# Optimization experiments

Hardware: AMD Instinct MI355X
Metric: run time of the kernel (lower is better)

The kernel has to match this reference:

```python
import jax, jax.numpy as jnp
import numpy as np

MAX_SIGMA = 10.0
TRUNCATE = 4.0
R = int(TRUNCATE * MAX_SIGMA + 0.5)  # 40, static max radius (scipy: int(truncate*sigma+0.5))
L = 2 * R + 1                         # 81


def _make_kernels(sigmas):
    # sigmas: [B] -> kernels [B, L], exactly matching scipy._gaussian_kernel1d
    pos = jnp.arange(-R, R + 1, dtype=sigmas.dtype)          # [L]
    r = jnp.floor(TRUNCATE * sigmas + 0.5)                   # per-sample radius
    w = jnp.exp(-0.5 * (pos[None, :] ** 2) / (sigmas[:, None] ** 2))
    w = w * (jnp.abs(pos)[None, :] <= r[:, None])            # scipy truncation
    return w / jnp.sum(w, axis=-1, keepdims=True)


def _reflect_index(n):
    # symmetric ('reflect' in scipy) boundary indices for pad width R, valid even if R > n
    i = jnp.arange(-R, n + R)
    j = jnp.mod(i, 2 * n)
    return jnp.where(j < n, j, 2 * n - 1 - j)


def _conv_last(x, k):
    # correlate along last axis with reflect boundary; x [..., n], k [L]
    n = x.shape[-1]
    xp = x[..., _reflect_index(n)]                            # [..., n+2R]
    flat = xp.reshape(-1, 1, n + 2 * R)
    out = jax.lax.conv_general_dilated(flat, k[None, None, :],
                                       window_strides=(1,), padding='VALID')
    return out.reshape(x.shape)


def _blur_one(xi, k):
    # xi: [C, H, W]; scipy gaussian_filter with scalar sigma blurs every axis
    for ax in range(xi.ndim):
        xi = jnp.moveaxis(_conv_last(jnp.moveaxis(xi, ax, -1), k), -1, ax)
    return xi


def setup_inputs() -> dict:
    key = jax.random.key(0)
    k1, _ = jax.random.split(key)
    B, C, H, W = 64, 3, 512, 512
    x = jax.random.uniform(k1, (B, C, H, W), dtype=jnp.float32)
    blur_sigmas = jnp.asarray(np.geomspace(0.5, MAX_SIGMA, 10), dtype=jnp.float32)
    fwd_steps = jax.random.randint(jax.random.fold_in(key, 1), (B,), 0, 10, dtype=jnp.int32)
    return {"x": x, "blur_sigmas": blur_sigmas, "fwd_steps": fwd_steps}


def reference(x, blur_sigmas, fwd_steps):
    sigmas = blur_sigmas[fwd_steps]          # [B]
    kernels = _make_kernels(sigmas)          # [B, L]
    return jax.vmap(_blur_one)(x, kernels)   # [B, C, H, W]
```

## Files before the change

kernel.cpp:

```cpp
#include <hip/hip_runtime.h>
#include <hip/hip_bf16.h>

#define RMAX 40
#define LK   81
#define HH   512
#define WW   512
#define CC   3
#define BB   64
#define ROWS 2

typedef unsigned short u16;
typedef __attribute__((ext_vector_type(8))) short short8;
typedef __attribute__((ext_vector_type(4))) float f32x4;

__device__ __forceinline__ u16 f2bf(float f) {
    unsigned u = __float_as_uint(f);
    u += 0x7FFFu + ((u >> 16) & 1u);
    return (u16)(u >> 16);
}
__device__ __forceinline__ float bf2f(u16 s) {
    return __uint_as_float(((unsigned)s) << 16);
}

__global__ __launch_bounds__(256) void prep_kernel(
    const float* __restrict__ sigmas10,
    const int*   __restrict__ steps,
    int*   __restrict__ rbuf,
    float* __restrict__ mbuf,
    float* __restrict__ wbuf,
    u16*   __restrict__ atab)
{
    const int b   = blockIdx.x;
    const int tid = threadIdx.x;
    const float sigma = sigmas10[steps[b]];
    int r = (int)floorf(4.0f * sigma + 0.5f);
    if (r > RMAX) r = RMAX;
    const float s2 = sigma * sigma;

    float sum = 0.0f;
    for (int p = -r; p <= r; ++p)
        sum += expf(-0.5f * (float)(p * p) / s2);
    const float inv = 1.0f / sum;

    if (tid < 128) {
        int p = tid - 56;
        float v = 0.0f;
        if (p >= -r && p <= r)
            v = expf(-0.5f * (float)(p * p) / s2) * inv;
        wbuf[b * 128 + tid] = v;
    }

    if (tid == 0) {
        rbuf[b] = r;
        float Mm[9];
        for (int i = 0; i < 9; ++i) Mm[i] = 0.0f;
        for (int p = -r; p <= r; ++p) {
            float wv = expf(-0.5f * (float)(p * p) / s2) * inv;
            for (int c = 0; c < CC; ++c) {
                int i = c + p;
                int j = ((i % 6) + 6) % 6;
                int cc = (j < 3) ? j : 5 - j;
                Mm[c * 3 + cc] += wv;
            }
        }
        for (int c = 0; c < 3; ++c)
            for (int cc = 0; cc < 3; ++cc)
                mbuf[b * 12 + c * 4 + cc] = Mm[c * 3 + cc];
    }

    u16* ab = atab + (size_t)b * 8192;
    int e = tid * 32;
    for (int ee = 0; ee < 32; ++ee, ++e) {
        int j    = e & 7;
        int lane = (e >> 3) & 63;
        int s    = e >> 9;
        int ch   = s >> 2;
        int half = (s >> 1) & 1;
        int prec = s & 1;
        int m = 32 * ch + ((lane >> 4) << 3) + j - (lane & 15) - 16 * half;
        float wfull = 0.0f;
        if (m >= 0 && m <= 2 * r) {
            int p = m - r;
            wfull = expf(-0.5f * (float)(p * p) / s2) * inv;
        }
        u16 hi = f2bf(wfull);
        u16 val = hi;
        if (prec) val = f2bf(wfull - bf2f(hi));
        ab[e] = val;
    }
}

__global__ __launch_bounds__(256) void passB_kernel(
    const float* __restrict__ x,
    const float* __restrict__ wbuf,
    const float* __restrict__ mbuf,
    const int*   __restrict__ rbuf,
    u16* __restrict__ out1)
{
    __shared__ __align__(16) float mixed[CC * ROWS][WW + 2 * RMAX];

    const int b   = blockIdx.y;
    const int h0  = blockIdx.x * ROWS;
    const int tid = threadIdx.x;
    const int r   = __builtin_amdgcn_readfirstlane(rbuf[b]);

    const float M00 = mbuf[b * 12 + 0], M01 = mbuf[b * 12 + 1], M02 = mbuf[b * 12 + 2];
    const float M10 = mbuf[b * 12 + 4], M11 = mbuf[b * 12 + 5], M12 = mbuf[b * 12 + 6];
    const float M20 = mbuf[b * 12 + 8], M21 = mbuf[b * 12 + 9], M22 = mbuf[b * 12 + 10];

    const float* xb = x + (size_t)b * CC * HH * WW + (size_t)h0 * WW;

    for (int idx = tid; idx < WW + 2 * RMAX; idx += 256) {
        int i  = idx - RMAX;
        int jm = i & (2 * WW - 1);
        int src = (jm < WW) ? jm : (2 * WW - 1 - jm);
        float a0 = __builtin_nontemporal_load(xb + src);
        float a1 = __builtin_nontemporal_load(xb + HH * WW + src);
        float a2 = __builtin_nontemporal_load(xb + 2 * HH * WW + src);
        float b0 = __builtin_nontemporal_load(xb + WW + src);
        float b1 = __builtin_nontemporal_load(xb + HH * WW + WW + src);
        float b2 = __builtin_nontemporal_load(xb + 2 * HH * WW + WW + src);
        mixed[0][idx] = M00 * a0 + M01 * a1 + M02 * a2;
        mixed[1][idx] = M00 * b0 + M01 * b1 + M02 * b2;
        mixed[2][idx] = M10 * a0 + M11 * a1 + M12 * a2;
        mixed[3][idx] = M10 * b0 + M11 * b1 + M12 * b2;
        mixed[4][idx] = M20 * a0 + M21 * a1 + M22 * a2;
        mixed[5][idx] = M20 * b0 + M21 * b1 + M22 * b2;
    }
    __syncthreads();

    const int t0    = (RMAX - r) & ~3;
    const int n4    = ((r + RMAX + 3 - t0) >> 2) + 1;
    const int kbase = (16 + t0) >> 2;
    const float4* K4 = (const float4*)(wbuf + b * 128);

#pragma unroll
    for (int k = 0; k < 3; ++k) {
        const int task = tid + 256 * k;
        const int g    = task & 127;
        const int rc   = task >> 7;
        const int w0   = g << 2;

        const int dbase = (w0 + t0) >> 2;
        const float4* D4 = (const float4*)(&mixed[rc][0]);

        float4 Wlo = K4[kbase - 1];
        float acc0 = 0.f, acc1 = 0.f, acc2 = 0.f, acc3 = 0.f;

        for (int s = 0; s < n4; ++s) {
            float4 Whi = K4[kbase + s];
            float4 D   = D4[dbase + s];
            acc0 += Whi.x * D.x; acc1 += Wlo.w * D.x; acc2 += Wlo.z * D.x; acc3 += Wlo.y * D.x;
            acc0 += Whi.y * D.y; acc1 += Whi.x * D.y; acc2 += Wlo.w * D.y; acc3 += Wlo.z * D.y;
            acc0 += Whi.z * D.z; acc1 += Whi.y * D.z; acc2 += Whi.x * D.z; acc3 += Wlo.w * D.z;
            acc0 += Whi.w * D.w; acc1 += Whi.z * D.w; acc2 += Whi.y * D.w; acc3 += Whi.x * D.w;
            Wlo = Whi;
        }

        ushort4 o;
        o.x = f2bf(acc0); o.y = f2bf(acc1); o.z = f2bf(acc2); o.w = f2bf(acc3);
        const int c = rc >> 1, row = rc & 1;
        u16* dst = out1 + ((size_t)b * CC + c) * HH * WW
                 + (size_t)(h0 + row) * WW + w0;
        *(ushort4*)dst = o;
    }
}

__device__ __forceinline__ int refl512(int i) {
    int jm = i & (2 * HH - 1);
    return (jm < HH) ? jm : (2 * HH - 1 - jm);
}

__global__ __launch_bounds__(256) void passC_kernel(
    const u16* __restrict__ in1,
    const u16* __restrict__ atab,
    const int* __restrict__ rbuf,
    float* __restrict__ out)
{
    const int tid  = threadIdx.x;
    const int lane = tid & 63;
    const int bc   = blockIdx.z;
    const int b    = bc / 3;
    const int r    = __builtin_amdgcn_readfirstlane(rbuf[b]);
    const int h0   = blockIdx.y * 32;
    const int w    = blockIdx.x * 64 + (tid >> 6) * 16 + (lane & 15);
    const int nch  = (2 * r + 63) >> 5;
    const int rowbase = h0 - r + ((lane >> 4) << 3);

    const u16* src = in1 + (size_t)bc * HH * WW + w;
    const short8* at = (const short8*)(atab + (size_t)b * 8192);

    f32x4 acc0 = {0.f, 0.f, 0.f, 0.f};
    f32x4 acc1 = {0.f, 0.f, 0.f, 0.f};

    for (int ch = 0; ch < nch; ++ch) {
        short8 bv;
#pragma unroll
        for (int j = 0; j < 8; ++j) {
            int row = refl512(rowbase + 32 * ch + j);
            bv[j] = (short)src[(size_t)row * WW];
        }
        short8 ah0 = at[(ch * 4 + 0) * 64 + lane];
        short8 al0 = at[(ch * 4 + 1) * 64 + lane];
        short8 ah1 = at[(ch * 4 + 2) * 64 + lane];
        short8 al1 = at[(ch * 4 + 3) * 64 + lane];

        acc0 = __builtin_amdgcn_mfma_f32_16x16x32_bf16(ah0, bv, acc0, 0, 0, 0);
        acc0 = __builtin_amdgcn_mfma_f32_16x16x32_bf16(al0, bv, acc0, 0, 0, 0);
        acc1 = __builtin_amdgcn_mfma_f32_16x16x32_bf16(ah1, bv, acc1, 0, 0, 0);
        acc1 = __builtin_amdgcn_mfma_f32_16x16x32_bf16(al1, bv, acc1, 0, 0, 0);
    }

    const int orow = h0 + ((lane >> 4) << 2);
    float* dst = out + (size_t)bc * HH * WW + (size_t)orow * WW + w;
#pragma unroll
    for (int q = 0; q < 4; ++q) {
        __builtin_nontemporal_store(acc0[q], dst + (size_t)q * WW);
        __builtin_nontemporal_store(acc1[q], dst + (size_t)(q + 16) * WW);
    }
}

extern "C" void kernel_launch(void* const* d_in, const int* in_sizes, int n_in,
                              void* d_out, int out_size, void* d_ws, size_t ws_size,
                              hipStream_t stream)
{
    const float* x      = (const float*)d_in[0];
    const float* sigmas = (const float*)d_in[1];
    const int*   steps  = (const int*)d_in[2];
    float*       out    = (float*)d_out;

    int*   rbuf  = (int*)d_ws;
    float* mbuf  = (float*)((char*)d_ws + 256);
    float* wbuf  = (float*)((char*)d_ws + 4096);
    u16*   atab  = (u16*)((char*)d_ws + 65536);
    u16*   inter = (u16*)((char*)d_ws + 65536 + (1 << 20));

    prep_kernel<<<64, 256, 0, stream>>>(sigmas, steps, rbuf, mbuf, wbuf, atab);

    dim3 gB(HH / ROWS, BB);
    passB_kernel<<<gB, 256, 0, stream>>>(x, wbuf, mbuf, rbuf, inter);

    dim3 gC(WW / 64, HH / 32, BB * CC);
    passC_kernel<<<gC, 256, 0, stream>>>(inter, atab, rbuf, out);
}
```

Before: 409.8 us.

## Use MFMA for horizontal pass and write transposed fp16 intermediate

Pass B's scalar FMA convolution along W becomes MFMA f16 matrix multiplies over an fp16 LDS tile of 16 rows, with XOR swizzling to avoid bank conflicts. It writes the intermediate transposed (W-major), so pass C can load 8 contiguous H samples with a single vector load instead of 8 strided gathers. The weight tables move from bf16 hi/lo split to f16 hi/lo, with the window start aligned to 8 via an offset. The risks are fp16 range and precision on the intermediate, and scattered 2-byte transposed stores in pass B.

```diff
diff --git a/kernel.cpp b/kernel.cpp
--- a/kernel.cpp
+++ b/kernel.cpp
@@ -2,32 +2,25 @@
 #include <hip/hip_bf16.h>
 
 #define RMAX 40
-#define LK   81
 #define HH   512
 #define WW   512
 #define CC   3
 #define BB   64
-#define ROWS 2
+#define HT   16
+#define LROW 640
 
 typedef unsigned short u16;
+typedef _Float16 half8 __attribute__((ext_vector_type(8)));
 typedef __attribute__((ext_vector_type(8))) short short8;
 typedef __attribute__((ext_vector_type(4))) float f32x4;
 
-__device__ __forceinline__ u16 f2bf(float f) {
-    unsigned u = __float_as_uint(f);
-    u += 0x7FFFu + ((u >> 16) & 1u);
-    return (u16)(u >> 16);
-}
-__device__ __forceinline__ float bf2f(u16 s) {
-    return __uint_as_float(((unsigned)s) << 16);
-}
+__device__ __forceinline__ u16 h2u(_Float16 h) { return __builtin_bit_cast(u16, h); }
 
 __global__ __launch_bounds__(256) void prep_kernel(
     const float* __restrict__ sigmas10,
     const int*   __restrict__ steps,
     int*   __restrict__ rbuf,
     float* __restrict__ mbuf,
-    float* __restrict__ wbuf,
     u16*   __restrict__ atab)
 {
     const int b   = blockIdx.x;
@@ -41,14 +34,6 @@
     for (int p = -r; p <= r; ++p)
         sum += expf(-0.5f * (float)(p * p) / s2);
     const float inv = 1.0f / sum;
-
-    if (tid < 128) {
-        int p = tid - 56;
-        float v = 0.0f;
-        if (p >= -r && p <= r)
-            v = expf(-0.5f * (float)(p * p) / s2) * inv;
-        wbuf[b * 128 + tid] = v;
-    }
 
     if (tid == 0) {
         rbuf[b] = r;
@@ -68,6 +53,7 @@
                 mbuf[b * 12 + c * 4 + cc] = Mm[c * 3 + cc];
     }
 
+    const int dlt = (-r) & 7;
     u16* ab = atab + (size_t)b * 8192;
     int e = tid * 32;
     for (int ee = 0; ee < 32; ++ee, ++e) {
@@ -77,30 +63,29 @@
         int ch   = s >> 2;
         int half = (s >> 1) & 1;
         int prec = s & 1;
-        int m = 32 * ch + ((lane >> 4) << 3) + j - (lane & 15) - 16 * half;
+        int m = 32 * ch + ((lane >> 4) << 3) + j - (lane & 15) - 16 * half - dlt;
         float wfull = 0.0f;
         if (m >= 0 && m <= 2 * r) {
             int p = m - r;
             wfull = expf(-0.5f * (float)(p * p) / s2) * inv;
         }
-        u16 hi = f2bf(wfull);
-        u16 val = hi;
-        if (prec) val = f2bf(wfull - bf2f(hi));
-        ab[e] = val;
-    }
-}
-
-__global__ __launch_bounds__(256) void passB_kernel(
+        _Float16 hi = (_Float16)wfull;
+        _Float16 val = prec ? (_Float16)(wfull - (float)hi) : hi;
+        ab[e] = h2u(val);
+    }
+}
+
+__global__ __launch_bounds__(512) void passB_kernel(
     const float* __restrict__ x,
-    const float* __restrict__ wbuf,
+    const u16*   __restrict__ atab,
     const float* __restrict__ mbuf,
     const int*   __restrict__ rbuf,
-    u16* __restrict__ out1)
-{
-    __shared__ __align__(16) float mixed[CC * ROWS][WW + 2 * RMAX];
+    u16* __restrict__ interT)
+{
+    __shared__ __align__(16) u16 mixs[CC][HT][LROW];
 
     const int b   = blockIdx.y;
-    const int h0  = blockIdx.x * ROWS;
+    const int h0  = blockIdx.x * HT;
     const int tid = threadIdx.x;
     const int r   = __builtin_amdgcn_readfirstlane(rbuf[b]);
 
@@ -110,59 +95,58 @@
 
     const float* xb = x + (size_t)b * CC * HH * WW + (size_t)h0 * WW;
 
-    for (int idx = tid; idx < WW + 2 * RMAX; idx += 256) {
-        int i  = idx - RMAX;
-        int jm = i & (2 * WW - 1);
+    for (int idx = tid; idx < HT * LROW; idx += 512) {
+        int h  = idx / LROW;
+        int wi = idx - h * LROW;
+        int lw = wi - RMAX;
+        int jm = lw & (2 * WW - 1);
         int src = (jm < WW) ? jm : (2 * WW - 1 - jm);
-        float a0 = __builtin_nontemporal_load(xb + src);
-        float a1 = __builtin_nontemporal_load(xb + HH * WW + src);
-        float a2 = __builtin_nontemporal_load(xb + 2 * HH * WW + src);
-        float b0 = __builtin_nontemporal_load(xb + WW + src);
-        float b1 = __builtin_nontemporal_load(xb + HH * WW + WW + src);
-        float b2 = __builtin_nontemporal_load(xb + 2 * HH * WW + WW + src);
-        mixed[0][idx] = M00 * a0 + M01 * a1 + M02 * a2;
-        mixed[1][idx] = M00 * b0 + M01 * b1 + M02 * b2;
-        mixed[2][idx] = M10 * a0 + M11 * a1 + M12 * a2;
-        mixed[3][idx] = M10 * b0 + M11 * b1 + M12 * b2;
-        mixed[4][idx] = M20 * a0 + M21 * a1 + M22 * a2;
-        mixed[5][idx] = M20 * b0 + M21 * b1 + M22 * b2;
+        const float* px = xb + (size_t)h * WW + src;
+        float a0 = __builtin_nontemporal_load(px);
+        float a1 = __builtin_nontemporal_load(px + HH * WW);
+        float a2 = __builtin_nontemporal_load(px + 2 * HH * WW);
+        int sw = wi ^ ((h & 7) << 3);
+        mixs[0][h][sw] = h2u((_Float16)(M00 * a0 + M01 * a1 + M02 * a2));
+        mixs[1][h][sw] = h2u((_Float16)(M10 * a0 + M11 * a1 + M12 * a2));
+        mixs[2][h][sw] = h2u((_Float16)(M20 * a0 + M21 * a1 + M22 * a2));
     }
     __syncthreads();
 
-    const int t0    = (RMAX - r) & ~3;
-    const int n4    = ((r + RMAX + 3 - t0) >> 2) + 1;
-    const int kbase = (16 + t0) >> 2;
-    const float4* K4 = (const float4*)(wbuf + b * 128);
-
+    const int dlt  = (-r) & 7;
+    const int nch  = (2 * r + dlt + 63) >> 5;
+    const int lane = tid & 63;
+    const int wv   = tid >> 6;
+    const int col  = lane & 15;
+    const int g    = lane >> 4;
+    const half8* at = (const half8*)(atab + (size_t)b * 8192);
+
+    for (int task = wv; task < 48; task += 8) {
+        const int c  = task >> 4;
+        const int w0 = (task & 15) << 5;
+        const int s0w = (w0 + RMAX - r) & ~7;
+        const u16* lrow = &mixs[c][col][0];
+
+        f32x4 acc0 = {0.f, 0.f, 0.f, 0.f};
+        f32x4 acc1 = {0.f, 0.f, 0.f, 0.f};
+        for (int ch = 0; ch < nch; ++ch) {
+            int wi = (s0w + 32 * ch + 8 * g) ^ ((col & 7) << 3);
+            half8 bv  = *(const half8*)(lrow + wi);
+            half8 ah0 = at[(ch * 4 + 0) * 64 + lane];
+            half8 al0 = at[(ch * 4 + 1) * 64 + lane];
+            half8 ah1 = at[(ch * 4 + 2) * 64 + lane];
+            half8 al1 = at[(ch * 4 + 3) * 64 + lane];
+            acc0 = __builtin_amdgcn_mfma_f32_16x16x32_f16(ah0, bv, acc0, 0, 0, 0);
+            acc0 = __builtin_amdgcn_mfma_f32_16x16x32_f16(al0, bv, acc0, 0, 0, 0);
+            acc1 = __builtin_amdgcn_mfma_f32_16x16x32_f16(ah1, bv, acc1, 0, 0, 0);
+            acc1 = __builtin_amdgcn_mfma_f32_16x16x32_f16(al1, bv, acc1, 0, 0, 0);
+        }
+        u16* orow = interT + (((size_t)b * CC + c) * WW + (w0 + 4 * g)) * HH
+                  + h0 + col;
 #pragma unroll
-    for (int k = 0; k < 3; ++k) {
-        const int task = tid + 256 * k;
-        const int g    = task & 127;
-        const int rc   = task >> 7;
-        const int w0   = g << 2;
-
-        const int dbase = (w0 + t0) >> 2;
-        const float4* D4 = (const float4*)(&mixed[rc][0]);
-
-        float4 Wlo = K4[kbase - 1];
-        float acc0 = 0.f, acc1 = 0.f, acc2 = 0.f, acc3 = 0.f;
-
-        for (int s = 0; s < n4; ++s) {
-            float4 Whi = K4[kbase + s];
-            float4 D   = D4[dbase + s];
-            acc0 += Whi.x * D.x; acc1 += Wlo.w * D.x; acc2 += Wlo.z * D.x; acc3 += Wlo.y * D.x;
-            acc0 += Whi.y * D.y; acc1 += Whi.x * D.y; acc2 += Wlo.w * D.y; acc3 += Wlo.z * D.y;
-            acc0 += Whi.z * D.z; acc1 += Whi.y * D.z; acc2 += Whi.x * D.z; acc3 += Wlo.w * D.z;
-            acc0 += Whi.w * D.w; acc1 += Whi.z * D.w; acc2 += Whi.y * D.w; acc3 += Whi.x * D.w;
-            Wlo = Whi;
-        }
-
-        ushort4 o;
-        o.x = f2bf(acc0); o.y = f2bf(acc1); o.z = f2bf(acc2); o.w = f2bf(acc3);
-        const int c = rc >> 1, row = rc & 1;
-        u16* dst = out1 + ((size_t)b * CC + c) * HH * WW
-                 + (size_t)(h0 + row) * WW + w0;
-        *(ushort4*)dst = o;
+        for (int q = 0; q < 4; ++q) {
+            orow[(size_t)q * HH]        = h2u((_Float16)acc0[q]);
+            orow[(size_t)(q + 16) * HH] = h2u((_Float16)acc1[q]);
+        }
     }
 }
 
@@ -172,7 +156,7 @@
 }
 
 __global__ __launch_bounds__(256) void passC_kernel(
-    const u16* __restrict__ in1,
+    const u16* __restrict__ interT,
     const u16* __restrict__ atab,
     const int* __restrict__ rbuf,
     float* __restrict__ out)
@@ -182,36 +166,41 @@
     const int bc   = blockIdx.z;
     const int b    = bc / 3;
     const int r    = __builtin_amdgcn_readfirstlane(rbuf[b]);
+    const int dlt  = (-r) & 7;
+    const int nch  = (2 * r + dlt + 63) >> 5;
     const int h0   = blockIdx.y * 32;
     const int w    = blockIdx.x * 64 + (tid >> 6) * 16 + (lane & 15);
-    const int nch  = (2 * r + 63) >> 5;
-    const int rowbase = h0 - r + ((lane >> 4) << 3);
-
-    const u16* src = in1 + (size_t)bc * HH * WW + w;
-    const short8* at = (const short8*)(atab + (size_t)b * 8192);
+    const int s0   = (h0 - r) & ~7;
+    const int g    = lane >> 4;
+
+    const u16* wrow = interT + ((size_t)bc * WW + w) * HH;
+    const half8* at = (const half8*)(atab + (size_t)b * 8192);
+    const bool fast = (s0 >= 0) && (s0 + 32 * nch <= HH);
 
     f32x4 acc0 = {0.f, 0.f, 0.f, 0.f};
     f32x4 acc1 = {0.f, 0.f, 0.f, 0.f};
 
     for (int ch = 0; ch < nch; ++ch) {
-        short8 bv;
+        short8 braw;
+        if (fast) {
+            braw = *(const short8*)(wrow + s0 + 32 * ch + 8 * g);
+        } else {
 #pragma unroll
-        for (int j = 0; j < 8; ++j) {
-            int row = refl512(rowbase + 32 * ch + j);
-            bv[j] = (short)src[(size_t)row * WW];
-        }
-        short8 ah0 = at[(ch * 4 + 0) * 64 + lane];
-        short8 al0 = at[(ch * 4 + 1) * 64 + lane];
-        short8 ah1 = at[(ch * 4 + 2) * 64 + lane];
-        short8 al1 = at[(ch * 4 + 3) * 64 + lane];
-
-        acc0 = __builtin_amdgcn_mfma_f32_16x16x32_bf16(ah0, bv, acc0, 0, 0, 0);
-        acc0 = __builtin_amdgcn_mfma_f32_16x16x32_bf16(al0, bv, acc0, 0, 0, 0);
-        acc1 = __builtin_amdgcn_mfma_f32_16x16x32_bf16(ah1, bv, acc1, 0, 0, 0);
-        acc1 = __builtin_amdgcn_mfma_f32_16x16x32_bf16(al1, bv, acc1, 0, 0, 0);
-    }
-
-    const int orow = h0 + ((lane >> 4) << 2);
+            for (int j = 0; j < 8; ++j)
+                braw[j] = (short)wrow[refl512(s0 + 32 * ch + 8 * g + j)];
+        }
+        half8 bv  = __builtin_bit_cast(half8, braw);
+        half8 ah0 = at[(ch * 4 + 0) * 64 + lane];
+        half8 al0 = at[(ch * 4 + 1) * 64 + lane];
+        half8 ah1 = at[(ch * 4 + 2) * 64 + lane];
+        half8 al1 = at[(ch * 4 + 3) * 64 + lane];
+        acc0 = __builtin_amdgcn_mfma_f32_16x16x32_f16(ah0, bv, acc0, 0, 0, 0);
+        acc0 = __builtin_amdgcn_mfma_f32_16x16x32_f16(al0, bv, acc0, 0, 0, 0);
+        acc1 = __builtin_amdgcn_mfma_f32_16x16x32_f16(ah1, bv, acc1, 0, 0, 0);
+        acc1 = __builtin_amdgcn_mfma_f32_16x16x32_f16(al1, bv, acc1, 0, 0, 0);
+    }
+
+    const int orow = h0 + 4 * g;
     float* dst = out + (size_t)bc * HH * WW + (size_t)orow * WW + w;
 #pragma unroll
     for (int q = 0; q < 4; ++q) {
@@ -229,17 +218,14 @@
     const int*   steps  = (const int*)d_in[2];
     float*       out    = (float*)d_out;
 
-    int*   rbuf  = (int*)d_ws;
-    float* mbuf  = (float*)((char*)d_ws + 256);
-    float* wbuf  = (float*)((char*)d_ws + 4096);
-    u16*   atab  = (u16*)((char*)d_ws + 65536);
-    u16*   inter = (u16*)((char*)d_ws + 65536 + (1 << 20));
-
-    prep_kernel<<<64, 256, 0, stream>>>(sigmas, steps, rbuf, mbuf, wbuf, atab);
-
-    dim3 gB(HH / ROWS, BB);
-    passB_kernel<<<gB, 256, 0, stream>>>(x, wbuf, mbuf, rbuf, inter);
-
-    dim3 gC(WW / 64, HH / 32, BB * CC);
-    passC_kernel<<<gC, 256, 0, stream>>>(inter, atab, rbuf, out);
-}
+    int*   rbuf   = (int*)d_ws;
+    float* mbuf   = (float*)((char*)d_ws + 256);
+    u16*   atab   = (u16*)((char*)d_ws + 4096);
+    u16*   interT = (u16*)((char*)d_ws + 4096 + (1 << 20));
+
+    prep_kernel<<<64, 256, 0, stream>>>(sigmas, steps, rbuf, mbuf, atab);
+
+    passB_kernel<<<dim3(HH / HT, BB), 512, 0, stream>>>(x, atab, mbuf, rbuf, interT);
+
+    passC_kernel<<<dim3(WW / 64, HH / 32, BB * CC), 256, 0, stream>>>(interT, atab, rbuf, out);
+}
```

After: 515.5 us. 25.8% more time.
